# Optimization experiments

Hardware: AMD Instinct MI355X
Metric: run time of the kernel (lower is better)

## Reference

```python
import jax, jax.numpy as jnp
import numpy as np

N = 512      # num_nodes
B = 32       # batch
T = 12       # encoder seq_len
HOR = 12     # decoder horizon
U = 64       # rnn_units
K = 2        # max_diffusion_step
M = 2 * K + 1  # num_matrices (2 supports)


def setup_inputs() -> dict:
    key = jax.random.key(0)
    ks = jax.random.split(key, 16)

    # dual random-walk supports: (D^-1 A)^T and (D^-1 A^T)^T, with self loops
    adj = (jax.random.uniform(ks[0], (N, N)) < 32.0 / N).astype(jnp.float32)

    def rw_T(a):
        a = a + jnp.eye(N, dtype=jnp.float32)
        return (a / a.sum(axis=1, keepdims=True)).T

    supports = jnp.stack([rw_T(adj), rw_T(adj.T)])  # (2, N, N)

    def w(k, shape, s=0.1):
        return jax.random.normal(k, shape, dtype=jnp.float32) * s

    Cin0 = (1 + U) * M   # layer0: input_dim(1)+units, times num_matrices
    Cin1 = (U + U) * M   # layer1
    return {
        "inputs": jax.random.normal(ks[1], (T, B, N * 1), dtype=jnp.float32),
        "supports": supports,
        "enc0_Wg": w(ks[2], (Cin0, 2 * U)), "enc0_bg": jnp.ones(2 * U, jnp.float32),
        "enc0_Wc": w(ks[3], (Cin0, U)),     "enc0_bc": jnp.zeros(U, jnp.float32),
        "enc1_Wg": w(ks[4], (Cin1, 2 * U)), "enc1_bg": jnp.ones(2 * U, jnp.float32),
        "enc1_Wc": w(ks[5], (Cin1, U)),     "enc1_bc": jnp.zeros(U, jnp.float32),
        "dec0_Wg": w(ks[6], (Cin0, 2 * U)), "dec0_bg": jnp.ones(2 * U, jnp.float32),
        "dec0_Wc": w(ks[7], (Cin0, U)),     "dec0_bc": jnp.zeros(U, jnp.float32),
        "dec1_Wg": w(ks[8], (Cin1, 2 * U)), "dec1_bg": jnp.ones(2 * U, jnp.float32),
        "dec1_Wc": w(ks[9], (Cin1, U)),     "dec1_bc": jnp.zeros(U, jnp.float32),
        "proj_W": w(ks[10], (U, 1)),        "proj_b": jnp.zeros(1, jnp.float32),
    }


def reference(inputs, supports, enc0_Wg, enc0_bg, enc0_Wc, enc0_bc,
              enc1_Wg, enc1_bg, enc1_Wc, enc1_bc,
              dec0_Wg, dec0_bg, dec0_Wc, dec0_bc,
              dec1_Wg, dec1_bg, dec1_Wc, dec1_bc, proj_W, proj_b):
    Bsz = inputs.shape[1]

    def gconv(x0, W, b):
        # x0: (B, N, C); Chebyshev-style diffusion over each support
        xs = [x0]
        for i in range(supports.shape[0]):
            s = supports[i]
            x1 = jnp.einsum('ij,bjc->bic', s, x0)
            xs.append(x1)
            xp, xpp = x1, x0
            for _ in range(K - 1):
                x2 = 2.0 * jnp.einsum('ij,bjc->bic', s, xp) - xpp
                xs.append(x2)
                xp, xpp = x2, xp
        # stack on last axis to match torch's (B,N,C,num_matrices) -> (B*N, C*M) layout
        z = jnp.stack(xs, axis=-1).reshape(Bsz, N, -1)
        return z @ W + b

    def cell(x, h, Wg, bg, Wc, bc):
        g = jax.nn.sigmoid(gconv(jnp.concatenate([x, h], axis=-1), Wg, bg))
        r, u = jnp.split(g, 2, axis=-1)
        c = jnp.tanh(gconv(jnp.concatenate([x, r * h], axis=-1), Wc, bc))
        return u * h + (1.0 - u) * c

    h0 = jnp.zeros((Bsz, N, U), inputs.dtype)
    h1 = jnp.zeros((Bsz, N, U), inputs.dtype)

    def enc_step(carry, xt):
        h0, h1 = carry
        x = xt.reshape(Bsz, N, 1)
        h0 = cell(x, h0, enc0_Wg, enc0_bg, enc0_Wc, enc0_bc)
        h1 = cell(h0, h1, enc1_Wg, enc1_bg, enc1_Wc, enc1_bc)
        return (h0, h1), None

    (h0, h1), _ = jax.lax.scan(enc_step, (h0, h1), inputs)

    def dec_step(carry, _):
        h0, h1, xin = carry
        h0 = cell(xin, h0, dec0_Wg, dec0_bg, dec0_Wc, dec0_bc)
        h1 = cell(h0, h1, dec1_Wg, dec1_bg, dec1_Wc, dec1_bc)
        out = h1 @ proj_W + proj_b        # (B, N, 1)
        return (h0, h1, out), out.reshape(Bsz, N)

    go = jnp.zeros((Bsz, N, 1), inputs.dtype)
    _, outs = jax.lax.scan(dec_step, (h0, h1, go), None, length=HOR)
    return outs  # (horizon, B, N*output_dim)
```

## Files before the change

### kernel.cpp

```cpp
#include <hip/hip_runtime.h>
#include <math.h>

#define NN 512
#define BB 32
#define TT 12
#define HH 12
#define UU 64
#define CAP 128
#define RTOT (NN * BB)

__device__ __forceinline__ float sigm(float x) { return 1.f / (1.f + expf(-x)); }

__global__ __launch_bounds__(256) void build_ell(const float* __restrict__ sup,
                                                 int2* __restrict__ ell8,
                                                 int2* __restrict__ ell4,
                                                 int* __restrict__ ecnt) {
    int wave = (blockIdx.x * blockDim.x + threadIdx.x) >> 6;
    int lane = threadIdx.x & 63;
    if (wave >= 2 * NN) return;
    const float* row = sup + (size_t)wave * NN;
    int base = 0;
    for (int k = 0; k < NN / 64; ++k) {
        float v = row[k * 64 + lane];
        unsigned long long m = __ballot(v != 0.0f);
        int pre = __popcll(m & ((1ull << lane) - 1ull));
        if (v != 0.0f) {
            int pos = base + pre;
            if (pos < CAP) {
                int j = k * 64 + lane;
                int vb = __float_as_int(v);
                ell8[(size_t)pos * 1024 + wave] = make_int2(j * 32 + (j & 1) * 16, vb);
                ell4[(size_t)pos * 1024 + wave] = make_int2(j * 16, vb);
            }
        }
        base += __popcll(m);
    }
    if (lane == 0) ecnt[wave] = base < CAP ? base : CAP;
}

__global__ void zero_kernel(float* __restrict__ p, int n) {
    int i = blockIdx.x * 256 + threadIdx.x;
    if (i < n) p[i] = 0.0f;
}

__global__ void wprep(const float* __restrict__ src, float* __restrict__ dstP,
                      float* __restrict__ dstX, int C, int OO, int WD, int L0) {
    int idx = blockIdx.x * 256 + threadIdx.x;
    int total = 5 * C * OO;
    if (idx >= total) return;
    int oi = idx % WD;
    int rem = idx / WD;
    int c = rem % C;
    int rem2 = rem / C;
    int m = rem2 % 5;
    int oq = rem2 / 5;
    int o = oq * WD + oi;
    int crow = L0 ? (c + 1) : c;
    size_t base = (size_t)crow * 5 * OO + o;
    float v;
    if (m == 0) v = src[base] - src[base + 2 * OO] - src[base + 4 * OO];
    else        v = src[base + (size_t)m * OO];
    dstP[idx] = v;
    if (L0 && c == 0) {
        size_t b0 = (size_t)o;
        float xvv;
        if (m == 0) xvv = src[b0] - src[b0 + 2 * OO] - src[b0 + 4 * OO];
        else        xvv = src[b0 + (size_t)m * OO];
        dstX[(oq * 5 + m) * WD + oi] = xvv;
    }
}

template<bool L0, bool GATE>
__global__ __launch_bounds__(512) void fused(const float* __restrict__ hA,
                                             const float* __restrict__ hB,
                                             const float* __restrict__ g,
                                             const float* __restrict__ Wp,
                                             const float* __restrict__ Xr,
                                             const float* __restrict__ xv,
                                             const float* __restrict__ bias,
                                             const int2* __restrict__ ell,
                                             const int* __restrict__ ecnt,
                                             float* __restrict__ gout,
                                             const float* __restrict__ hOld,
                                             float* __restrict__ hNew) {
    constexpr int C  = L0 ? 64 : 128;
    constexpr int WD = GATE ? 8 : 4;

    __shared__ float S[512 * WD * 2];
    float* T0 = S;
    float* T1 = S + 512 * WD;

    int bid = blockIdx.x;
    int swz = (bid & 7) * 64 + (bid >> 3);
    int b = swz >> 4, oq = swz & 15;
    int o0 = oq * WD;
    int n = threadIdx.x;
    int cnt0 = ecnt[n], cnt1 = ecnt[NN + n];
    float xn = L0 ? xv[b * 512 + n] : 0.f;

    const float* Wb = Wp + (size_t)oq * 5 * C * WD;
    float acc[5][WD];
    #pragma unroll
    for (int oi = 0; oi < WD; ++oi) acc[0][oi] = bias[o0 + oi];
    #pragma unroll
    for (int m = 1; m < 5; ++m)
        #pragma unroll
        for (int oi = 0; oi < WD; ++oi) acc[m][oi] = 0.f;

    #pragma unroll 2
    for (int c = 0; c < C; ++c) {
        float a;
        if (L0) {
            if (GATE) a = hA[(size_t)((b << 6) + c) * 512 + n];
            else      a = g[(size_t)((b << 7) + c) * 512 + n];
        } else {
            if (c < 64) {
                a = hA[(size_t)((b << 6) + c) * 512 + n];
            } else {
                int u = c - 64;
                if (GATE) a = hB[(size_t)((b << 6) + u) * 512 + n];
                else      a = g[(size_t)((b << 7) + u) * 512 + n];
            }
        }
        #pragma unroll
        for (int m = 0; m < 5; ++m) {
            const float* wrow = Wb + ((size_t)m * C + c) * WD;
            #pragma unroll
            for (int oi = 0; oi < WD; ++oi)
                acc[m][oi] += a * wrow[oi];
        }
    }

    if (L0) {
        const float* xr = Xr + (size_t)oq * 5 * WD;
        #pragma unroll
        for (int m = 0; m < 5; ++m)
            #pragma unroll
            for (int oi = 0; oi < WD; ++oi)
                acc[m][oi] += xn * xr[m * WD + oi];
    }

    float uval[WD], hval[WD];
    if (!GATE) {
        #pragma unroll
        for (int oi = 0; oi < WD; ++oi) {
            uval[oi] = g[(size_t)((b << 7) + 64 + o0 + oi) * 512 + n];
            hval[oi] = hOld[(size_t)((b << 6) + o0 + oi) * 512 + n];
        }
    }

    if constexpr (WD == 8) {
        *(float4*)&T0[n * 8 + (n & 1) * 4] =
            make_float4(acc[2][0], acc[2][1], acc[2][2], acc[2][3]);
        *(float4*)&T0[n * 8 + ((n & 1) ^ 1) * 4] =
            make_float4(acc[2][4], acc[2][5], acc[2][6], acc[2][7]);
        *(float4*)&T1[n * 8 + (n & 1) * 4] =
            make_float4(acc[4][0], acc[4][1], acc[4][2], acc[4][3]);
        *(float4*)&T1[n * 8 + ((n & 1) ^ 1) * 4] =
            make_float4(acc[4][4], acc[4][5], acc[4][6], acc[4][7]);
    } else {
        *(float4*)&T0[n * 4] = make_float4(acc[2][0], acc[2][1], acc[2][2], acc[2][3]);
        *(float4*)&T1[n * 4] = make_float4(acc[4][0], acc[4][1], acc[4][2], acc[4][3]);
    }

    auto gather = [&](const float* T, int s, float* o) {
        int cnt = s ? cnt1 : cnt0;
        const int2* e0 = ell + s * NN + n;
        const char* Tbyte = (const char*)T;
        float a0[WD];
        #pragma unroll
        for (int i = 0; i < WD; ++i) a0[i] = 0.f;
        #pragma unroll 2
        for (int p = 0; p < cnt; ++p) {
            int2 e = e0[(size_t)p << 10];
            float v = __int_as_float(e.y);
            if constexpr (WD == 8) {
                float4 x0 = *(const float4*)(Tbyte + e.x);
                float4 x1 = *(const float4*)(Tbyte + (e.x ^ 16));
                a0[0] += v * x0.x; a0[1] += v * x0.y; a0[2] += v * x0.z; a0[3] += v * x0.w;
                a0[4] += v * x1.x; a0[5] += v * x1.y; a0[6] += v * x1.z; a0[7] += v * x1.w;
            } else {
                float4 x0 = *(const float4*)(Tbyte + e.x);
                a0[0] += v * x0.x; a0[1] += v * x0.y; a0[2] += v * x0.z; a0[3] += v * x0.w;
            }
        }
        #pragma unroll
        for (int i = 0; i < WD; ++i) o[i] = a0[i];
    };
    auto put = [&](float* T, const float* y) {
        if constexpr (WD == 8) {
            *(float4*)&T[n * 8 + (n & 1) * 4]       = make_float4(y[0], y[1], y[2], y[3]);
            *(float4*)&T[n * 8 + ((n & 1) ^ 1) * 4] = make_float4(y[4], y[5], y[6], y[7]);
        } else {
            *(float4*)&T[n * 4] = make_float4(y[0], y[1], y[2], y[3]);
        }
    };

    float g2[WD], g4[WD], t1[WD];

    __syncthreads();

    gather(T0, 0, t1);
    #pragma unroll
    for (int oi = 0; oi < WD; ++oi) acc[1][oi] += 2.f * t1[oi];
    gather(T1, 1, t1);
    #pragma unroll
    for (int oi = 0; oi < WD; ++oi) acc[3][oi] += 2.f * t1[oi];

    __syncthreads();

    put(T0, acc[1]);
    put(T1, acc[3]);

    __syncthreads();

    gather(T0, 0, g2);
    gather(T1, 1, g4);

    #pragma unroll
    for (int oi = 0; oi < WD; ++oi) {
        float accf = acc[0][oi] + g2[oi] + g4[oi];
        if (GATE) {
            float s = sigm(accf);
            if (oq < 8) {
                const float* hG = L0 ? hA : hB;
                float hv = hG[(size_t)((b << 6) + o0 + oi) * 512 + n];
                gout[(size_t)((b << 7) + o0 + oi) * 512 + n] = s * hv;
            } else {
                gout[(size_t)((b << 7) + o0 + oi) * 512 + n] = s;
            }
        } else {
            float cv = tanhf(accf);
            hNew[(size_t)((b << 6) + o0 + oi) * 512 + n] =
                uval[oi] * hval[oi] + (1.f - uval[oi]) * cv;
        }
    }
}

__global__ void proj_kernel(const float* __restrict__ h1, const float* __restrict__ pW,
                            const float* __restrict__ pb, float* __restrict__ outt) {
    int r = blockIdx.x * 256 + threadIdx.x;
    if (r >= RTOT) return;
    int b = r >> 9, n = r & 511;
    float acc = pb[0];
    #pragma unroll 16
    for (int u = 0; u < 64; ++u)
        acc += h1[(size_t)((b << 6) + u) * 512 + n] * pW[u];
    outt[b * NN + n] = acc;
}

extern "C" void kernel_launch(void* const* d_in, const int* in_sizes, int n_in,
                              void* d_out, int out_size, void* d_ws, size_t ws_size,
                              hipStream_t stream) {
    const float* inputs   = (const float*)d_in[0];
    const float* supports = (const float*)d_in[1];
    const float* enc0_Wg = (const float*)d_in[2];
    const float* enc0_bg = (const float*)d_in[3];
    const float* enc0_Wc = (const float*)d_in[4];
    const float* enc0_bc = (const float*)d_in[5];
    const float* enc1_Wg = (const float*)d_in[6];
    const float* enc1_bg = (const float*)d_in[7];
    const float* enc1_Wc = (const float*)d_in[8];
    const float* enc1_bc = (const float*)d_in[9];
    const float* dec0_Wg = (const float*)d_in[10];
    const float* dec0_bg = (const float*)d_in[11];
    const float* dec0_Wc = (const float*)d_in[12];
    const float* dec0_bc = (const float*)d_in[13];
    const float* dec1_Wg = (const float*)d_in[14];
    const float* dec1_bg = (const float*)d_in[15];
    const float* dec1_Wc = (const float*)d_in[16];
    const float* dec1_bc = (const float*)d_in[17];
    const float* projW   = (const float*)d_in[18];
    const float* projb   = (const float*)d_in[19];
    float* out = (float*)d_out;

    char* wsb = (char*)d_ws;
    size_t off = 0;
    auto alloc = [&](size_t bytes) -> char* {
        char* p = wsb + off;
        off = (off + bytes + 255) & ~(size_t)255;
        return p;
    };
    int2*  ell8  = (int2*)alloc((size_t)CAP * 1024 * 8);
    int2*  ell4  = (int2*)alloc((size_t)CAP * 1024 * 8);
    int*   ecnt  = (int*)alloc((size_t)2 * NN * 4);
    float* h0a   = (float*)alloc((size_t)RTOT * UU * 4);
    float* h1a   = (float*)alloc((size_t)RTOT * UU * 4);
    float* xzero = (float*)alloc((size_t)RTOT * 4);
    float* h0b   = (float*)alloc((size_t)RTOT * UU * 4);
    float* h1b   = (float*)alloc((size_t)RTOT * UU * 4);
    float* g     = (float*)alloc((size_t)RTOT * 128 * 4);
    float* p_e0g = (float*)alloc((size_t)5 * 64 * 128 * 4);
    float* x_e0g = (float*)alloc((size_t)16 * 5 * 8 * 4);
    float* p_e0c = (float*)alloc((size_t)5 * 64 * 64 * 4);
    float* x_e0c = (float*)alloc((size_t)16 * 5 * 4 * 4);
    float* p_e1g = (float*)alloc((size_t)5 * 128 * 128 * 4);
    float* p_e1c = (float*)alloc((size_t)5 * 128 * 64 * 4);
    float* p_d0g = (float*)alloc((size_t)5 * 64 * 128 * 4);
    float* x_d0g = (float*)alloc((size_t)16 * 5 * 8 * 4);
    float* p_d0c = (float*)alloc((size_t)5 * 64 * 64 * 4);
    float* x_d0c = (float*)alloc((size_t)16 * 5 * 4 * 4);
    float* p_d1g = (float*)alloc((size_t)5 * 128 * 128 * 4);
    float* p_d1c = (float*)alloc((size_t)5 * 128 * 64 * 4);
    float* xdum  = (float*)alloc((size_t)16 * 5 * 8 * 4);
    if (off > ws_size) return;

    build_ell<<<256, 256, 0, stream>>>(supports, ell8, ell4, ecnt);
    {
        int nz = RTOT * UU * 2 + RTOT;
        zero_kernel<<<(nz + 255) / 256, 256, 0, stream>>>(h0a, nz);
    }
    wprep<<<(5 * 64 * 128 + 255) / 256, 256, 0, stream>>>(enc0_Wg, p_e0g, x_e0g, 64, 128, 8, 1);
    wprep<<<(5 * 64 * 64 + 255) / 256, 256, 0, stream>>>(enc0_Wc, p_e0c, x_e0c, 64, 64, 4, 1);
    wprep<<<(5 * 128 * 128 + 255) / 256, 256, 0, stream>>>(enc1_Wg, p_e1g, xdum, 128, 128, 8, 0);
    wprep<<<(5 * 128 * 64 + 255) / 256, 256, 0, stream>>>(enc1_Wc, p_e1c, xdum, 128, 64, 4, 0);
    wprep<<<(5 * 64 * 128 + 255) / 256, 256, 0, stream>>>(dec0_Wg, p_d0g, x_d0g, 64, 128, 8, 1);
    wprep<<<(5 * 64 * 64 + 255) / 256, 256, 0, stream>>>(dec0_Wc, p_d0c, x_d0c, 64, 64, 4, 1);
    wprep<<<(5 * 128 * 128 + 255) / 256, 256, 0, stream>>>(dec1_Wg, p_d1g, xdum, 128, 128, 8, 0);
    wprep<<<(5 * 128 * 64 + 255) / 256, 256, 0, stream>>>(dec1_Wc, p_d1c, xdum, 128, 64, 4, 0);

    float *h0c = h0a, *h0n = h0b, *h1c = h1a, *h1n = h1b;

    auto cell_l0 = [&](const float* x_bn, const float* Wg_, const float* Xg_,
                       const float* bg_, const float* Wc_, const float* Xc_,
                       const float* bc_) {
        fused<true, true><<<512, 512, 0, stream>>>(h0c, nullptr, g, Wg_, Xg_, x_bn,
                                                   bg_, ell8, ecnt, g, nullptr, nullptr);
        fused<true, false><<<512, 512, 0, stream>>>(h0c, nullptr, g, Wc_, Xc_, x_bn,
                                                    bc_, ell4, ecnt, nullptr, h0c, h0n);
        float* t = h0c; h0c = h0n; h0n = t;
    };
    auto cell_l1 = [&](const float* Wg_, const float* bg_,
                       const float* Wc_, const float* bc_) {
        fused<false, true><<<512, 512, 0, stream>>>(h0c, h1c, g, Wg_, nullptr, nullptr,
                                                    bg_, ell8, ecnt, g, nullptr, nullptr);
        fused<false, false><<<512, 512, 0, stream>>>(h0c, h1c, g, Wc_, nullptr, nullptr,
                                                     bc_, ell4, ecnt, nullptr, h1c, h1n);
        float* t = h1c; h1c = h1n; h1n = t;
    };

    for (int t = 0; t < TT; ++t) {
        cell_l0(inputs + (size_t)t * BB * NN, p_e0g, x_e0g, enc0_bg, p_e0c, x_e0c, enc0_bc);
        cell_l1(p_e1g, enc1_bg, p_e1c, enc1_bc);
    }
    for (int t = 0; t < HH; ++t) {
        const float* xin = (t == 0) ? xzero : (out + (size_t)(t - 1) * BB * NN);
        cell_l0(xin, p_d0g, x_d0g, dec0_bg, p_d0c, x_d0c, dec0_bc);
        cell_l1(p_d1g, dec1_bg, p_d1c, dec1_bc);
        proj_kernel<<<(RTOT + 255) / 256, 256, 0, stream>>>(h1c, projW, projb,
                                                            out + (size_t)t * BB * NN);
    }
}
```

Baseline: 4.794 ms.

## Interleave sparse LDS gathers with dense weight FMAs across diffusion phases

Splits the dense projection into three passes (matrices 2/4 first, then 1/3, then 0). The sparse neighbor gathers from LDS are interleaved into the later dense loops so that gather latency overlaps with global loads and FMAs, and fewer accumulators stay live at once. The cost is reloading the input activations three times and adding branchy control flow in the inner loop.

```diff
diff --git a/kernel.cpp b/kernel.cpp
--- a/kernel.cpp
+++ b/kernel.cpp
@@ -83,8 +83,9 @@
                                              float* __restrict__ gout,
                                              const float* __restrict__ hOld,
                                              float* __restrict__ hNew) {
-    constexpr int C  = L0 ? 64 : 128;
-    constexpr int WD = GATE ? 8 : 4;
+    constexpr int C    = L0 ? 64 : 128;
+    constexpr int WD   = GATE ? 8 : 4;
+    constexpr int STEP = L0 ? 2 : 3;
 
     __shared__ float S[512 * WD * 2];
     float* T0 = S;
@@ -99,93 +100,31 @@
     float xn = L0 ? xv[b * 512 + n] : 0.f;
 
     const float* Wb = Wp + (size_t)oq * 5 * C * WD;
-    float acc[5][WD];
-    #pragma unroll
-    for (int oi = 0; oi < WD; ++oi) acc[0][oi] = bias[o0 + oi];
-    #pragma unroll
-    for (int m = 1; m < 5; ++m)
-        #pragma unroll
-        for (int oi = 0; oi < WD; ++oi) acc[m][oi] = 0.f;
-
-    #pragma unroll 2
-    for (int c = 0; c < C; ++c) {
-        float a;
+    const float* xr = Xr + (size_t)oq * 5 * WD;
+    const int2* e00 = ell + n;
+    const int2* e01 = ell + NN + n;
+
+    auto loadA = [&](int c) -> float {
         if (L0) {
-            if (GATE) a = hA[(size_t)((b << 6) + c) * 512 + n];
-            else      a = g[(size_t)((b << 7) + c) * 512 + n];
+            if (GATE) return hA[(size_t)((b << 6) + c) * 512 + n];
+            else      return g[(size_t)((b << 7) + c) * 512 + n];
         } else {
-            if (c < 64) {
-                a = hA[(size_t)((b << 6) + c) * 512 + n];
-            } else {
-                int u = c - 64;
-                if (GATE) a = hB[(size_t)((b << 6) + u) * 512 + n];
-                else      a = g[(size_t)((b << 7) + u) * 512 + n];
-            }
-        }
-        #pragma unroll
-        for (int m = 0; m < 5; ++m) {
-            const float* wrow = Wb + ((size_t)m * C + c) * WD;
-            #pragma unroll
-            for (int oi = 0; oi < WD; ++oi)
-                acc[m][oi] += a * wrow[oi];
-        }
-    }
-
-    if (L0) {
-        const float* xr = Xr + (size_t)oq * 5 * WD;
-        #pragma unroll
-        for (int m = 0; m < 5; ++m)
-            #pragma unroll
-            for (int oi = 0; oi < WD; ++oi)
-                acc[m][oi] += xn * xr[m * WD + oi];
-    }
-
-    float uval[WD], hval[WD];
-    if (!GATE) {
-        #pragma unroll
-        for (int oi = 0; oi < WD; ++oi) {
-            uval[oi] = g[(size_t)((b << 7) + 64 + o0 + oi) * 512 + n];
-            hval[oi] = hOld[(size_t)((b << 6) + o0 + oi) * 512 + n];
-        }
-    }
-
-    if constexpr (WD == 8) {
-        *(float4*)&T0[n * 8 + (n & 1) * 4] =
-            make_float4(acc[2][0], acc[2][1], acc[2][2], acc[2][3]);
-        *(float4*)&T0[n * 8 + ((n & 1) ^ 1) * 4] =
-            make_float4(acc[2][4], acc[2][5], acc[2][6], acc[2][7]);
-        *(float4*)&T1[n * 8 + (n & 1) * 4] =
-            make_float4(acc[4][0], acc[4][1], acc[4][2], acc[4][3]);
-        *(float4*)&T1[n * 8 + ((n & 1) ^ 1) * 4] =
-            make_float4(acc[4][4], acc[4][5], acc[4][6], acc[4][7]);
-    } else {
-        *(float4*)&T0[n * 4] = make_float4(acc[2][0], acc[2][1], acc[2][2], acc[2][3]);
-        *(float4*)&T1[n * 4] = make_float4(acc[4][0], acc[4][1], acc[4][2], acc[4][3]);
-    }
-
-    auto gather = [&](const float* T, int s, float* o) {
-        int cnt = s ? cnt1 : cnt0;
-        const int2* e0 = ell + s * NN + n;
-        const char* Tbyte = (const char*)T;
-        float a0[WD];
-        #pragma unroll
-        for (int i = 0; i < WD; ++i) a0[i] = 0.f;
-        #pragma unroll 2
-        for (int p = 0; p < cnt; ++p) {
-            int2 e = e0[(size_t)p << 10];
-            float v = __int_as_float(e.y);
-            if constexpr (WD == 8) {
-                float4 x0 = *(const float4*)(Tbyte + e.x);
-                float4 x1 = *(const float4*)(Tbyte + (e.x ^ 16));
-                a0[0] += v * x0.x; a0[1] += v * x0.y; a0[2] += v * x0.z; a0[3] += v * x0.w;
-                a0[4] += v * x1.x; a0[5] += v * x1.y; a0[6] += v * x1.z; a0[7] += v * x1.w;
-            } else {
-                float4 x0 = *(const float4*)(Tbyte + e.x);
-                a0[0] += v * x0.x; a0[1] += v * x0.y; a0[2] += v * x0.z; a0[3] += v * x0.w;
-            }
-        }
-        #pragma unroll
-        for (int i = 0; i < WD; ++i) o[i] = a0[i];
+            if (c < 64) return hA[(size_t)((b << 6) + c) * 512 + n];
+            int u = c - 64;
+            if (GATE) return hB[(size_t)((b << 6) + u) * 512 + n];
+            else      return g[(size_t)((b << 7) + u) * 512 + n];
+        }
+    };
+    auto gstep = [&](const float* T, const int2* e0, int p, float* t) {
+        int2 e = e0[(size_t)p << 10];
+        float v = __int_as_float(e.y);
+        const char* Tb = (const char*)T;
+        float4 x0 = *(const float4*)(Tb + e.x);
+        t[0] += v * x0.x; t[1] += v * x0.y; t[2] += v * x0.z; t[3] += v * x0.w;
+        if constexpr (WD == 8) {
+            float4 x1 = *(const float4*)(Tb + (e.x ^ 16));
+            t[4] += v * x1.x; t[5] += v * x1.y; t[6] += v * x1.z; t[7] += v * x1.w;
+        }
     };
     auto put = [&](float* T, const float* y) {
         if constexpr (WD == 8) {
@@ -196,30 +135,106 @@
         }
     };
 
-    float g2[WD], g4[WD], t1[WD];
+    float acc2[WD], acc4[WD];
+    #pragma unroll
+    for (int oi = 0; oi < WD; ++oi) { acc2[oi] = 0.f; acc4[oi] = 0.f; }
+    #pragma unroll 4
+    for (int c = 0; c < C; ++c) {
+        float a = loadA(c);
+        const float* w2 = Wb + ((size_t)2 * C + c) * WD;
+        const float* w4 = Wb + ((size_t)4 * C + c) * WD;
+        #pragma unroll
+        for (int oi = 0; oi < WD; ++oi) acc2[oi] += a * w2[oi];
+        #pragma unroll
+        for (int oi = 0; oi < WD; ++oi) acc4[oi] += a * w4[oi];
+    }
+    if (L0) {
+        #pragma unroll
+        for (int oi = 0; oi < WD; ++oi) acc2[oi] += xn * xr[2 * WD + oi];
+        #pragma unroll
+        for (int oi = 0; oi < WD; ++oi) acc4[oi] += xn * xr[4 * WD + oi];
+    }
+    put(T0, acc2);
+    put(T1, acc4);
+
+    float uval[WD], hval[WD];
+    if (!GATE) {
+        #pragma unroll
+        for (int oi = 0; oi < WD; ++oi) {
+            uval[oi] = g[(size_t)((b << 7) + 64 + o0 + oi) * 512 + n];
+            hval[oi] = hOld[(size_t)((b << 6) + o0 + oi) * 512 + n];
+        }
+    }
 
     __syncthreads();
 
-    gather(T0, 0, t1);
-    #pragma unroll
-    for (int oi = 0; oi < WD; ++oi) acc[1][oi] += 2.f * t1[oi];
-    gather(T1, 1, t1);
-    #pragma unroll
-    for (int oi = 0; oi < WD; ++oi) acc[3][oi] += 2.f * t1[oi];
+    float acc1[WD], acc3[WD], t1[WD], t2[WD];
+    #pragma unroll
+    for (int oi = 0; oi < WD; ++oi) { acc1[oi] = 0.f; acc3[oi] = 0.f; t1[oi] = 0.f; t2[oi] = 0.f; }
+    {
+        int p1 = 0, p2 = 0, slot = 0;
+        for (int c = 0; c < C; ++c) {
+            float a = loadA(c);
+            const float* w1 = Wb + ((size_t)1 * C + c) * WD;
+            const float* w3 = Wb + ((size_t)3 * C + c) * WD;
+            #pragma unroll
+            for (int oi = 0; oi < WD; ++oi) acc1[oi] += a * w1[oi];
+            #pragma unroll
+            for (int oi = 0; oi < WD; ++oi) acc3[oi] += a * w3[oi];
+            if (slot == 0) {
+                if (p1 < cnt0) { gstep(T0, e00, p1, t1); ++p1; }
+                if (p2 < cnt1) { gstep(T1, e01, p2, t2); ++p2; }
+            }
+            if (++slot == STEP) slot = 0;
+        }
+        for (; p1 < cnt0; ++p1) gstep(T0, e00, p1, t1);
+        for (; p2 < cnt1; ++p2) gstep(T1, e01, p2, t2);
+    }
+    if (L0) {
+        #pragma unroll
+        for (int oi = 0; oi < WD; ++oi) acc1[oi] += xn * xr[1 * WD + oi];
+        #pragma unroll
+        for (int oi = 0; oi < WD; ++oi) acc3[oi] += xn * xr[3 * WD + oi];
+    }
+    #pragma unroll
+    for (int oi = 0; oi < WD; ++oi) acc1[oi] += 2.f * t1[oi];
+    #pragma unroll
+    for (int oi = 0; oi < WD; ++oi) acc3[oi] += 2.f * t2[oi];
 
     __syncthreads();
 
-    put(T0, acc[1]);
-    put(T1, acc[3]);
+    put(T0, acc1);
+    put(T1, acc3);
 
     __syncthreads();
 
-    gather(T0, 0, g2);
-    gather(T1, 1, g4);
+    float acc0[WD];
+    #pragma unroll
+    for (int oi = 0; oi < WD; ++oi) { acc0[oi] = bias[o0 + oi]; t1[oi] = 0.f; t2[oi] = 0.f; }
+    {
+        int p1 = 0, p2 = 0, slot = 0;
+        for (int c = 0; c < C; ++c) {
+            float a = loadA(c);
+            const float* w0 = Wb + (size_t)c * WD;
+            #pragma unroll
+            for (int oi = 0; oi < WD; ++oi) acc0[oi] += a * w0[oi];
+            if (slot == 0) {
+                if (p1 < cnt0) { gstep(T0, e00, p1, t1); ++p1; }
+                if (p2 < cnt1) { gstep(T1, e01, p2, t2); ++p2; }
+            }
+            if (++slot == STEP) slot = 0;
+        }
+        for (; p1 < cnt0; ++p1) gstep(T0, e00, p1, t1);
+        for (; p2 < cnt1; ++p2) gstep(T1, e01, p2, t2);
+    }
+    if (L0) {
+        #pragma unroll
+        for (int oi = 0; oi < WD; ++oi) acc0[oi] += xn * xr[0 * WD + oi];
+    }
 
     #pragma unroll
     for (int oi = 0; oi < WD; ++oi) {
-        float accf = acc[0][oi] + g2[oi] + g4[oi];
+        float accf = acc0[oi] + t1[oi] + t2[oi];
         if (GATE) {
             float s = sigm(accf);
             if (oq < 8) {
```

Result: slower. 6.887 ms (+43.7%).
